# Kernel optimization log

Measured on AMD Instinct MI355X. Metric: run time of the kernel, lower is better.

The kernel has to match this reference:

```python
import jax, jax.numpy as jnp
import numpy as np

B, T, I, H, K, C, TH, CLS = 128, 512, 300, 150, 6, 300, 20, 5

def setup_inputs() -> dict:
    key = jax.random.key(0)
    ks = jax.random.split(key, 16)
    s = lambda *sh: 1.0 / np.sqrt(sh[-1])
    inp = {
        "x": jax.random.normal(ks[0], (B, T, I), jnp.float32),
        # GRU params (PyTorch layout: [3H, in]) for fwd/bwd directions
        "Wih_f": jax.random.normal(ks[1], (3 * H, I), jnp.float32) * s(3 * H, I),
        "Whh_f": jax.random.normal(ks[2], (3 * H, H), jnp.float32) * s(3 * H, H),
        "bih_f": jax.random.normal(ks[3], (3 * H,), jnp.float32) * 0.01,
        "bhh_f": jax.random.normal(ks[4], (3 * H,), jnp.float32) * 0.01,
        "Wih_b": jax.random.normal(ks[5], (3 * H, I), jnp.float32) * s(3 * H, I),
        "Whh_b": jax.random.normal(ks[6], (3 * H, H), jnp.float32) * s(3 * H, H),
        "bih_b": jax.random.normal(ks[7], (3 * H,), jnp.float32) * 0.01,
        "bhh_b": jax.random.normal(ks[8], (3 * H,), jnp.float32) * 0.01,
        # topic attention params (stacked over K topics)
        "attn_context": jax.random.normal(ks[9], (K, C), jnp.float32),
        "Wattn": jax.random.normal(ks[10], (K, C + 2 * H, 2 * H), jnp.float32) * s(1, C + 2 * H),
        "battn": jax.random.normal(ks[11], (K, 2 * H), jnp.float32) * 0.01,
        "Wtop": jax.random.normal(ks[12], (K, 2 * H, TH), jnp.float32) * s(1, 2 * H),
        "btop": jax.random.normal(ks[13], (K, TH), jnp.float32) * 0.01,
        "Wout": jax.random.normal(ks[14], (K * TH, CLS), jnp.float32) * s(1, K * TH),
        "bout": jax.random.normal(ks[15], (CLS,), jnp.float32) * 0.01,
    }
    return inp

def _gru_dir(x, Wih, Whh, bih, bhh, reverse):
    # x: [B,T,I] -> outputs [B,T,H], final hidden [B,H]
    xT = jnp.swapaxes(x, 0, 1)                    # [T,B,I]
    if reverse:
        xT = xT[::-1]
    gi = xT @ Wih.T + bih                         # [T,B,3H] input projections (one big GEMM)
    h0 = jnp.zeros((x.shape[0], Whh.shape[1]), x.dtype)
    def step(h, g):
        gh = h @ Whh.T + bhh
        i_r, i_z, i_n = jnp.split(g, 3, axis=-1)
        h_r, h_z, h_n = jnp.split(gh, 3, axis=-1)
        r = jax.nn.sigmoid(i_r + h_r)
        z = jax.nn.sigmoid(i_z + h_z)
        n = jnp.tanh(i_n + r * h_n)
        h_new = (1.0 - z) * n + z * h
        return h_new, h_new
    hT, ys = jax.lax.scan(step, h0, gi)
    if reverse:
        ys = ys[::-1]
    return jnp.swapaxes(ys, 0, 1), hT

def reference(x, Wih_f, Whh_f, bih_f, bhh_f, Wih_b, Whh_b, bih_b, bhh_b,
              attn_context, Wattn, battn, Wtop, btop, Wout, bout):
    # eval mode: dropout is identity
    out_f, h_f = _gru_dir(x, Wih_f, Whh_f, bih_f, bhh_f, False)
    out_b, h_b = _gru_dir(x, Wih_b, Whh_b, bih_b, bhh_b, True)
    seq = jnp.concatenate([out_f, out_b], axis=-1)       # [B,T,2H]
    hidden = jnp.concatenate([h_f, h_b], axis=-1)        # [B,2H]
    Bsz = x.shape[0]
    Kt = attn_context.shape[0]
    # per-topic context: cat(context_k, hidden) -> linear -> tanh, batched over topics
    ctx_in = jnp.concatenate([
        jnp.broadcast_to(attn_context[None, :, :], (Bsz, Kt, attn_context.shape[1])),
        jnp.broadcast_to(hidden[:, None, :], (Bsz, Kt, hidden.shape[1])),
    ], axis=-1)                                          # [B,K,C+2H]
    context = jnp.tanh(jnp.einsum('bkc,kcd->bkd', ctx_in, Wattn) + battn)  # [B,K,2H]
    # attention pooling over time, all topics at once
    energy = jnp.einsum('btd,bkd->btk', seq, context)    # [B,T,K]
    probs = jax.nn.softmax(energy, axis=1)
    pooled = jnp.einsum('btd,btk->bkd', seq, probs)      # [B,K,2H]
    topic = jax.nn.relu(jnp.einsum('bkd,kdh->bkh', pooled, Wtop) + btop)   # [B,K,TH]
    feats = topic.reshape(Bsz, -1)                       # [B,K*TH]
    logits = feats @ Wout + bout
    out = jax.nn.softmax(logits, axis=1)                 # eval + validate=False path
    # regularization loss on normalized contexts
    nc = context / jnp.linalg.norm(context, axis=2, keepdims=True).clip(1e-12)
    G = jnp.einsum('bkd,bjd->bkj', nc, nc)               # [B,K,K]
    diff = G - jnp.eye(Kt, dtype=G.dtype)[None]
    reg = jnp.mean(jnp.sqrt(jnp.sum(diff * diff, axis=(1, 2))))
    return out, reg
```

## Files before the change

kernel.cpp:

```cpp
#include <hip/hip_runtime.h>
#include <hip/hip_bf16.h>
#include <math.h>

#define Bq   128
#define Tq   512
#define Iq   300
#define Hq   150
#define G3   450
#define Kq   6
#define Cq   300
#define D2   300
#define THq  20
#define CLSq 5

typedef __attribute__((ext_vector_type(8))) short short8;
typedef __attribute__((ext_vector_type(4))) float floatx4;

__global__ __launch_bounds__(256) void cast_bf16_kernel(
    const float* __restrict__ in, __hip_bfloat16* __restrict__ out, int n4)
{
    const int i = blockIdx.x * 256 + threadIdx.x;
    if (i < n4) {
        float4 v = *(const float4*)(in + 4 * (size_t)i);
        out[4 * (size_t)i + 0] = __float2bfloat16(v.x);
        out[4 * (size_t)i + 1] = __float2bfloat16(v.y);
        out[4 * (size_t)i + 2] = __float2bfloat16(v.z);
        out[4 * (size_t)i + 3] = __float2bfloat16(v.w);
    }
}

#define LB 40

__global__ __launch_bounds__(256) void gi_gemm_mfma(
    const __hip_bfloat16* __restrict__ xb,
    const __hip_bfloat16* __restrict__ Wbf,
    const float* __restrict__ bf_, const float* __restrict__ bb_,
    float* __restrict__ gic, int t0f, int t0b, int tcShift)
{
    const int dir = blockIdx.z;
    const unsigned short* W = (const unsigned short*)(Wbf + (size_t)dir * G3 * Iq);
    const unsigned short* X = (const unsigned short*)xb;
    const float* bias = dir ? bb_ : bf_;
    const int t0 = dir ? t0b : t0f;
    const int TCr = 1 << tcShift;
    float* outb = gic + (size_t)dir * Bq * TCr * G3;

    const int m0 = blockIdx.y * 128;
    const int n0 = blockIdx.x * 128;
    const int tid  = threadIdx.x;
    const int wv   = tid >> 6, lane = tid & 63;
    const int wm   = wv & 1,  wn   = wv >> 1;
    const int quad = lane >> 4, mr = lane & 15;

    __shared__ __align__(16) unsigned short Ab[128 * LB];
    __shared__ __align__(16) unsigned short Bb[128 * LB];

    floatx4 acc[4][4];
    #pragma unroll
    for (int i = 0; i < 4; ++i)
        #pragma unroll
        for (int j = 0; j < 4; ++j)
            acc[i][j] = (floatx4){0.f, 0.f, 0.f, 0.f};

    for (int k0 = 0; k0 < 320; k0 += 32) {
        __syncthreads();
        #pragma unroll
        for (int i = 0; i < 4; ++i) {
            const int g = tid + 256 * i;
            const int row = g >> 3, kq = g & 7;
            const int k = k0 + kq * 4;
            const int r = m0 + row;
            const int bb2 = r >> tcShift, lt = r & (TCr - 1);
            ushort4 av = make_ushort4(0, 0, 0, 0);
            if (k < Iq)
                av = *(const ushort4*)(X + ((size_t)bb2 * Tq + t0 + lt) * Iq + k);
            *(ushort4*)&Ab[row * LB + kq * 4] = av;
            const int n = n0 + row;
            ushort4 bv = make_ushort4(0, 0, 0, 0);
            if (n < G3 && k < Iq)
                bv = *(const ushort4*)(W + (size_t)n * Iq + k);
            *(ushort4*)&Bb[row * LB + kq * 4] = bv;
        }
        __syncthreads();

        short8 af[4], bfr[4];
        #pragma unroll
        for (int i = 0; i < 4; ++i)
            af[i] = *(const short8*)&Ab[(wm * 64 + i * 16 + mr) * LB + quad * 8];
        #pragma unroll
        for (int j = 0; j < 4; ++j)
            bfr[j] = *(const short8*)&Bb[(wn * 64 + j * 16 + mr) * LB + quad * 8];
        #pragma unroll
        for (int i = 0; i < 4; ++i)
            #pragma unroll
            for (int j = 0; j < 4; ++j)
                acc[i][j] = __builtin_amdgcn_mfma_f32_16x16x32_bf16(
                    af[i], bfr[j], acc[i][j], 0, 0, 0);
    }

    #pragma unroll
    for (int j = 0; j < 4; ++j) {
        const int gn = n0 + wn * 64 + j * 16 + mr;
        if (gn >= G3) continue;
        const float bv = bias[gn];
        #pragma unroll
        for (int i = 0; i < 4; ++i) {
            const int mbase = m0 + wm * 64 + i * 16 + quad * 4;
            #pragma unroll
            for (int rg = 0; rg < 4; ++rg)
                outb[(size_t)(mbase + rg) * G3 + gn] = acc[i][j][rg] + bv;
        }
    }
}

__global__ __launch_bounds__(512, 2) void gru_rec(
    const float* __restrict__ gic,
    const float* __restrict__ Whh_f, const float* __restrict__ bhh_f,
    const float* __restrict__ Whh_b, const float* __restrict__ bhh_b,
    float* __restrict__ hstate,
    float* __restrict__ seq,
    int chunk, int tcShift)
{
    const int TCr = 1 << tcShift;
    const int bid = blockIdx.x;
    const int dir = bid & 1;
    const int b   = bid >> 1;
    const float* Whh = dir ? Whh_b : Whh_f;
    const float* bhh = dir ? bhh_b : bhh_f;
    const int tid = threadIdx.x;
    const int rq  = tid >> 2;
    const int p   = tid & 3;
    const bool gact = (rq < 113);
    const bool iact = (tid < 450);

    __shared__ __align__(16) float stage[64 * 150];
    __shared__ __align__(16) float4 hbuf4[40];
    __shared__ __align__(16) float ghp[4][456];
    __shared__ float gi_s[456];
    float* hbuf = (float*)hbuf4;

    float w[4][40];

    for (int c = 0; c < 8; ++c) {
        const int r0 = c * 64;
        const int nrows = (r0 + 64 <= G3) ? 64 : (G3 - r0);
        const int nel = nrows * 150;
        __syncthreads();
        for (int idx = tid * 4; idx < nel; idx += 512 * 4)
            *(float4*)&stage[idx] = *(const float4*)(Whh + (size_t)r0 * 150 + idx);
        __syncthreads();
        if (gact && (rq >> 4) == c) {
            const int rl = 4 * rq - r0;
            const int cmax = (p == 3) ? 36 : 38;
            #pragma unroll
            for (int r = 0; r < 4; ++r) {
                const bool rv = (4 * rq + r < G3);
                #pragma unroll
                for (int cc = 0; cc < 40; ++cc)
                    w[r][cc] = (rv && cc < cmax)
                             ? stage[(rl + r) * 150 + p * 38 + cc] : 0.f;
            }
        }
    }

    float bh3[3] = {0.f, 0.f, 0.f};
    if (tid < Hq) {
        bh3[0] = bhh[tid];
        bh3[1] = bhh[150 + tid];
        bh3[2] = bhh[300 + tid];
    }
    const int hslot = (tid / 38) * 40 + (tid % 38);

    float* hs = hstate + (size_t)(dir * Bq + b) * Hq;
    if (tid < 160) {
        const int pp = tid / 40, off = tid % 40;
        const int j = pp * 38 + off;
        hbuf[tid] = (off < 38 && j < Hq && chunk > 0) ? hs[j] : 0.f;
    }
    __syncthreads();

    const float* gib = gic + (size_t)(dir * Bq + b) * TCr * G3;
    const int t0 = dir ? (Tq - TCr * (chunk + 1)) : (chunk * TCr);
    float* seqb = seq + (size_t)b * Tq * D2 + dir * Hq;

    int lt = dir ? (TCr - 1) : 0;
    float gval = iact ? gib[(size_t)lt * G3 + tid] : 0.f;

    for (int s = 0; s < TCr; ++s) {
        const int ltn = dir ? (TCr - 2 - s) : (s + 1);
        float gnext = 0.f;
        if (s + 1 < TCr && iact)
            gnext = gib[(size_t)ltn * G3 + tid];

        if (iact) gi_s[tid] = gval;

        if (gact) {
            const float4* hh = hbuf4 + p * 10;
            float acc0 = 0.f, acc1 = 0.f, acc2 = 0.f, acc3 = 0.f;
            #pragma unroll
            for (int q = 0; q < 10; ++q) {
                const float4 hv = hh[q];
                acc0 += hv.x * w[0][4*q]   + hv.y * w[0][4*q+1]
                      + hv.z * w[0][4*q+2] + hv.w * w[0][4*q+3];
                acc1 += hv.x * w[1][4*q]   + hv.y * w[1][4*q+1]
                      + hv.z * w[1][4*q+2] + hv.w * w[1][4*q+3];
                acc2 += hv.x * w[2][4*q]   + hv.y * w[2][4*q+1]
                      + hv.z * w[2][4*q+2] + hv.w * w[2][4*q+3];
                acc3 += hv.x * w[3][4*q]   + hv.y * w[3][4*q+1]
                      + hv.z * w[3][4*q+2] + hv.w * w[3][4*q+3];
            }
            *(float4*)&ghp[p][4 * rq] = make_float4(acc0, acc1, acc2, acc3);
        }
        __syncthreads();

        if (tid < Hq) {
            const float ghr = ghp[0][tid] + ghp[1][tid]
                            + ghp[2][tid] + ghp[3][tid] + bh3[0];
            const float ghz = ghp[0][150+tid] + ghp[1][150+tid]
                            + ghp[2][150+tid] + ghp[3][150+tid] + bh3[1];
            const float ghn = ghp[0][300+tid] + ghp[1][300+tid]
                            + ghp[2][300+tid] + ghp[3][300+tid] + bh3[2];
            const float r = 1.f / (1.f + __expf(-(gi_s[tid]       + ghr)));
            const float z = 1.f / (1.f + __expf(-(gi_s[150 + tid] + ghz)));
            const float nv = tanhf(gi_s[300 + tid] + r * ghn);
            const float hn = (1.f - z) * nv + z * hbuf[hslot];
            hbuf[hslot] = hn;
            stage[(s & 63) * 150 + tid] = hn;
        }
        __syncthreads();

        if ((s & 63) == 63 || s == TCr - 1) {
            const int sf0 = s & ~63;
            const int nf2 = (s - sf0 + 1) * 75;
            for (int idx = tid; idx < nf2; idx += 512) {
                const int rrow = idx / 75, cc = idx % 75;
                const int ss = sf0 + rrow;
                const int ltw = dir ? (TCr - 1 - ss) : ss;
                *(float2*)(seqb + (size_t)(t0 + ltw) * D2 + 2 * cc) =
                    *(const float2*)&stage[rrow * 150 + 2 * cc];
            }
        }

        gval = gnext;
        lt = ltn;
    }

    if (tid < Hq) hs[tid] = hbuf[hslot];
}

__global__ void ctxw_kernel(
    const float* __restrict__ attn_context,
    const float* __restrict__ Wattn,
    const float* __restrict__ battn,
    float* __restrict__ ctxW)
{
    const int o = blockIdx.x * 256 + threadIdx.x;
    if (o >= Kq * D2) return;
    const int k = o / D2, d = o % D2;
    float acc = battn[o];
    const float* Wp = Wattn + ((size_t)k * (Cq + D2)) * D2 + d;
    for (int c = 0; c < Cq; ++c)
        acc += attn_context[k * Cq + c] * Wp[(size_t)c * D2];
    ctxW[o] = acc;
}

__global__ __launch_bounds__(256) void ctx_compute(
    const float* __restrict__ seq,
    const float* __restrict__ Wattn,
    const float* __restrict__ ctxW,
    float* __restrict__ context,
    float* __restrict__ normsq)
{
    const int b = blockIdx.x;
    const int k = blockIdx.y;
    const int tid = threadIdx.x;
    const int lane = tid & 63, wv = tid >> 6;

    __shared__ float hb[304];
    __shared__ float red[4];

    for (int i = tid; i < D2; i += 256)
        hb[i] = (i < Hq) ? seq[((size_t)b * Tq + (Tq - 1)) * D2 + i]
                         : seq[(size_t)b * Tq * D2 + i];
    __syncthreads();

    float ssq = 0.f;
    for (int d = tid; d < D2; d += 256) {
        float acc = ctxW[k * D2 + d];
        const float* Wp = Wattn + ((size_t)k * (Cq + D2) + Cq) * D2 + d;
        for (int jj = 0; jj < D2; ++jj)
            acc += hb[jj] * Wp[(size_t)jj * D2];
        const float c = tanhf(acc);
        context[((size_t)b * Kq + k) * D2 + d] = c;
        ssq += c * c;
    }
    for (int off = 32; off > 0; off >>= 1) ssq += __shfl_xor(ssq, off, 64);
    if (lane == 0) red[wv] = ssq;
    __syncthreads();
    if (tid == 0) normsq[b * Kq + k] = red[0] + red[1] + red[2] + red[3];
}

__global__ __launch_bounds__(256) void gram_kernel(
    const float* __restrict__ context,
    const float* __restrict__ normsq,
    float* __restrict__ regbuf)
{
    const int b = blockIdx.x;
    const int tid = threadIdx.x;
    __shared__ float ctx[Kq * D2];
    __shared__ float Gm[36];

    for (int o = tid; o < Kq * D2; o += 256)
        ctx[o] = context[(size_t)b * Kq * D2 + o];
    __syncthreads();

    if (tid < 36) {
        const int k = tid / 6, jj = tid % 6;
        float g = 0.f;
        for (int d = 0; d < D2; ++d)
            g += ctx[k * D2 + d] * ctx[jj * D2 + d];
        const float nk = fmaxf(sqrtf(normsq[b * Kq + k]), 1e-12f);
        const float nj = fmaxf(sqrtf(normsq[b * Kq + jj]), 1e-12f);
        g /= (nk * nj);
        const float diff = g - ((k == jj) ? 1.f : 0.f);
        Gm[tid] = diff * diff;
    }
    __syncthreads();
    if (tid == 0) {
        float s = 0.f;
        for (int i = 0; i < 36; ++i) s += Gm[i];
        regbuf[b] = sqrtf(s);
    }
}

__global__ __launch_bounds__(256) void energy_kernel(
    const float* __restrict__ seq,
    const float* __restrict__ context,
    float* __restrict__ en)
{
    const int tc = blockIdx.x;
    const int b  = blockIdx.y;
    const int tid = threadIdx.x;
    const int lane = tid & 63, wv = tid >> 6;

    __shared__ float ctx[Kq * D2];
    for (int o = tid; o < Kq * D2; o += 256)
        ctx[o] = context[(size_t)b * Kq * D2 + o];
    __syncthreads();

    const float* seqb = seq + (size_t)b * Tq * D2;
    for (int s = 0; s < 16; ++s) {
        const int tt = tc * 64 + s * 4 + wv;
        float acc[Kq] = {0.f,0.f,0.f,0.f,0.f,0.f};
        for (int d = lane; d < D2; d += 64) {
            const float sv = seqb[(size_t)tt * D2 + d];
            #pragma unroll
            for (int k = 0; k < Kq; ++k) acc[k] += sv * ctx[k * D2 + d];
        }
        #pragma unroll
        for (int k = 0; k < Kq; ++k) {
            float v = acc[k];
            for (int off = 32; off > 0; off >>= 1) v += __shfl_xor(v, off, 64);
            if (lane == 0) en[((size_t)b * Tq + tt) * Kq + k] = v;
        }
    }
}

__global__ __launch_bounds__(256) void softmax_kernel(float* __restrict__ en)
{
    const int b = blockIdx.x;
    const int tid = threadIdx.x;
    const int lane = tid & 63, wv = tid >> 6;
    __shared__ float es[Tq * Kq];
    __shared__ float red[8];

    for (int o = tid; o < Tq * Kq; o += 256)
        es[o] = en[(size_t)b * Tq * Kq + o];
    __syncthreads();

    for (int k = 0; k < Kq; ++k) {
        float m = -1e30f;
        for (int tt = tid; tt < Tq; tt += 256) m = fmaxf(m, es[tt * Kq + k]);
        for (int off = 32; off > 0; off >>= 1) m = fmaxf(m, __shfl_xor(m, off, 64));
        if (lane == 0) red[wv] = m;
        __syncthreads();
        m = fmaxf(fmaxf(red[0], red[1]), fmaxf(red[2], red[3]));
        float ssum = 0.f;
        for (int tt = tid; tt < Tq; tt += 256) {
            const float e = __expf(es[tt * Kq + k] - m);
            es[tt * Kq + k] = e;
            ssum += e;
        }
        for (int off = 32; off > 0; off >>= 1) ssum += __shfl_xor(ssum, off, 64);
        if (lane == 0) red[4 + wv] = ssum;
        __syncthreads();
        const float inv = 1.f / (red[4] + red[5] + red[6] + red[7]);
        for (int tt = tid; tt < Tq; tt += 256) es[tt * Kq + k] *= inv;
        __syncthreads();
    }

    for (int o = tid; o < Tq * Kq; o += 256)
        en[(size_t)b * Tq * Kq + o] = es[o];
}

__global__ __launch_bounds__(256) void pooledp_kernel(
    const float* __restrict__ seq,
    const float* __restrict__ en,
    float* __restrict__ partial)
{
    const int tc = blockIdx.x;
    const int b  = blockIdx.y;
    const int tid = threadIdx.x;
    const int lane = tid & 63, wv = tid >> 6;

    __shared__ float pr[64 * Kq];
    __shared__ float part[4][Kq * D2];

    if (tid < 64 * Kq / 2) {
        pr[tid]       = en[((size_t)b * Tq + tc * 64) * Kq + tid];
        pr[tid + 192] = en[((size_t)b * Tq + tc * 64) * Kq + tid + 192];
    }
    __syncthreads();

    const float* seqb = seq + (size_t)b * Tq * D2;

    float pp[Kq][5];
    #pragma unroll
    for (int k = 0; k < Kq; ++k)
        #pragma unroll
        for (int q = 0; q < 5; ++q) pp[k][q] = 0.f;

    for (int s = 0; s < 16; ++s) {
        const int tl = s * 4 + wv;
        const int tt = tc * 64 + tl;
        float prr[Kq];
        #pragma unroll
        for (int k = 0; k < Kq; ++k) prr[k] = pr[tl * Kq + k];
        #pragma unroll
        for (int q = 0; q < 5; ++q) {
            const int d = lane + q * 64;
            const float sv = (d < D2) ? seqb[(size_t)tt * D2 + d] : 0.f;
            #pragma unroll
            for (int k = 0; k < Kq; ++k) pp[k][q] += prr[k] * sv;
        }
    }
    #pragma unroll
    for (int k = 0; k < Kq; ++k)
        #pragma unroll
        for (int q = 0; q < 5; ++q) {
            const int d = lane + q * 64;
            if (d < D2) part[wv][k * D2 + d] = pp[k][q];
        }
    __syncthreads();
    float* op = partial + ((size_t)b * 8 + tc) * (Kq * D2);
    for (int o = tid; o < Kq * D2; o += 256)
        op[o] = part[0][o] + part[1][o] + part[2][o] + part[3][o];
}

__global__ __launch_bounds__(256) void final_kernel(
    const float* __restrict__ partial,
    const float* __restrict__ Wtop,
    const float* __restrict__ btop,
    const float* __restrict__ Wout,
    const float* __restrict__ bout,
    float* __restrict__ outp)
{
    const int b = blockIdx.x;
    const int tid = threadIdx.x;
    __shared__ float pooled[Kq * D2];
    __shared__ float feats[Kq * THq];
    __shared__ float lsm[8];

    for (int o = tid; o < Kq * D2; o += 256) {
        float s = 0.f;
        #pragma unroll
        for (int c = 0; c < 8; ++c)
            s += partial[((size_t)b * 8 + c) * (Kq * D2) + o];
        pooled[o] = s;
    }
    __syncthreads();

    if (tid < Kq * THq) {
        const int k = tid / THq, hh = tid % THq;
        float acc = btop[tid];
        const float* wp = Wtop + (size_t)k * D2 * THq + hh;
        for (int d = 0; d < D2; ++d)
            acc += pooled[k * D2 + d] * wp[(size_t)d * THq];
        feats[tid] = fmaxf(acc, 0.f);
    }
    __syncthreads();

    if (tid < CLSq) {
        float acc = bout[tid];
        for (int f = 0; f < Kq * THq; ++f)
            acc += feats[f] * Wout[f * CLSq + tid];
        lsm[tid] = acc;
    }
    __syncthreads();
    if (tid < CLSq) {
        float m = lsm[0];
        for (int c = 1; c < CLSq; ++c) m = fmaxf(m, lsm[c]);
        float s = 0.f;
        for (int c = 0; c < CLSq; ++c) s += __expf(lsm[c] - m);
        outp[(size_t)b * CLSq + tid] = __expf(lsm[tid] - m) / s;
    }
}

__global__ void reg_final(const float* __restrict__ regbuf, float* __restrict__ outp)
{
    const int tid = threadIdx.x;
    float v = regbuf[tid];
    for (int off = 32; off > 0; off >>= 1) v += __shfl_xor(v, off, 64);
    __shared__ float r2[2];
    if ((tid & 63) == 0) r2[tid >> 6] = v;
    __syncthreads();
    if (tid == 0) outp[Bq * CLSq] = (r2[0] + r2[1]) * (1.f / (float)Bq);
}

extern "C" void kernel_launch(void* const* d_in, const int* in_sizes, int n_in,
                              void* d_out, int out_size, void* d_ws, size_t ws_size,
                              hipStream_t stream)
{
    const float* x     = (const float*)d_in[0];
    const float* Wih_f = (const float*)d_in[1];
    const float* Whh_f = (const float*)d_in[2];
    const float* bih_f = (const float*)d_in[3];
    const float* bhh_f = (const float*)d_in[4];
    const float* Wih_b = (const float*)d_in[5];
    const float* Whh_b = (const float*)d_in[6];
    const float* bih_b = (const float*)d_in[7];
    const float* bhh_b = (const float*)d_in[8];
    const float* attn_context = (const float*)d_in[9];
    const float* Wattn = (const float*)d_in[10];
    const float* battn = (const float*)d_in[11];
    const float* Wtop  = (const float*)d_in[12];
    const float* btop  = (const float*)d_in[13];
    const float* Wout  = (const float*)d_in[14];
    const float* bout  = (const float*)d_in[15];
    float* outp = (float*)d_out;

    float* ws       = (float*)d_ws;
    float* seqv     = ws;
    float* hstate   = seqv + (size_t)Bq * Tq * D2;
    float* ctxW     = hstate + (size_t)2 * Bq * Hq;
    float* context  = ctxW + Kq * D2;
    float* regbuf   = context + (size_t)Bq * Kq * D2;
    float* normsq   = regbuf + Bq;
    float* en       = normsq + Bq * Kq;
    float* partial  = en + (size_t)Bq * Tq * Kq;
    __hip_bfloat16* xb16 = (__hip_bfloat16*)(partial + (size_t)Bq * 8 * Kq * D2);
    __hip_bfloat16* Wb16 = xb16 + (size_t)Bq * Tq * Iq;
    float* gi_chunk = (float*)(Wb16 + (size_t)2 * G3 * Iq);
    const size_t fixed_floats = (size_t)(gi_chunk - ws);

    int tcShift = 5;
    for (int sh = 8; sh >= 5; --sh) {
        size_t need = (fixed_floats + (size_t)115200 * (1 << sh)) * 4;
        if (need <= ws_size) { tcShift = sh; break; }
    }
    const int TCr = 1 << tcShift;
    const int NL = Tq / TCr;

    cast_bf16_kernel<<<dim3((Bq * Tq * Iq / 4 + 255) / 256), 256, 0, stream>>>(
        x, xb16, Bq * Tq * Iq / 4);
    cast_bf16_kernel<<<dim3((G3 * Iq / 4 + 255) / 256), 256, 0, stream>>>(
        Wih_f, Wb16, G3 * Iq / 4);
    cast_bf16_kernel<<<dim3((G3 * Iq / 4 + 255) / 256), 256, 0, stream>>>(
        Wih_b, Wb16 + (size_t)G3 * Iq, G3 * Iq / 4);

    for (int c = 0; c < NL; ++c) {
        const int t0f = c * TCr;
        const int t0b = Tq - TCr * (c + 1);
        gi_gemm_mfma<<<dim3(4, Bq * TCr / 128, 2), 256, 0, stream>>>(
            xb16, Wb16, bih_f, bih_b, gi_chunk, t0f, t0b, tcShift);
        gru_rec<<<dim3(2 * Bq), 512, 0, stream>>>(
            gi_chunk, Whh_f, bhh_f, Whh_b, bhh_b, hstate, seqv, c, tcShift);
    }

    ctxw_kernel<<<dim3((Kq * D2 + 255) / 256), 256, 0, stream>>>(
        attn_context, Wattn, battn, ctxW);
    ctx_compute<<<dim3(Bq, Kq), 256, 0, stream>>>(seqv, Wattn, ctxW, context, normsq);
    gram_kernel<<<dim3(Bq), 256, 0, stream>>>(context, normsq, regbuf);
    energy_kernel<<<dim3(8, Bq), 256, 0, stream>>>(seqv, context, en);
    softmax_kernel<<<dim3(Bq), 256, 0, stream>>>(en);
    pooledp_kernel<<<dim3(8, Bq), 256, 0, stream>>>(seqv, en, partial);
    final_kernel<<<dim3(Bq), 256, 0, stream>>>(partial, Wtop, btop, Wout, bout, outp);
    reg_final<<<dim3(1), 128, 0, stream>>>(regbuf, outp);
}
```

Before: 1.047 ms.

## Fuse bf16 cast into GEMM loads, use fp16 dot2 recurrence with burst gi prefetch

Removes the separate bf16 cast kernels and converts x and Wih to bf16 while loading them inside the MFMA GEMM. In the recurrent kernel, Whh is held in registers as packed fp16 pairs and the hidden state is mirrored in fp16 so the matvec uses fdot2, halving register weight storage and the FMA count. Input-gate projections are now prefetched into shared memory in double-buffered bursts of 8 timesteps instead of one per-step global load, and the seq flush granularity drops to 32 steps. The fp16 hidden state and weights reduce accuracy in the recurrence, and the extra shared memory may affect occupancy.

```diff
diff --git a/kernel.cpp b/kernel.cpp
--- a/kernel.cpp
+++ b/kernel.cpp
@@ -15,31 +15,33 @@
 
 typedef __attribute__((ext_vector_type(8))) short short8;
 typedef __attribute__((ext_vector_type(4))) float floatx4;
-
-__global__ __launch_bounds__(256) void cast_bf16_kernel(
-    const float* __restrict__ in, __hip_bfloat16* __restrict__ out, int n4)
-{
-    const int i = blockIdx.x * 256 + threadIdx.x;
-    if (i < n4) {
-        float4 v = *(const float4*)(in + 4 * (size_t)i);
-        out[4 * (size_t)i + 0] = __float2bfloat16(v.x);
-        out[4 * (size_t)i + 1] = __float2bfloat16(v.y);
-        out[4 * (size_t)i + 2] = __float2bfloat16(v.z);
-        out[4 * (size_t)i + 3] = __float2bfloat16(v.w);
-    }
+typedef __attribute__((ext_vector_type(2))) _Float16 half2_t;
+
+static __device__ __forceinline__ unsigned short f2bf(float f) {
+    unsigned int u = __builtin_bit_cast(unsigned int, f);
+    u += 0x7FFFu + ((u >> 16) & 1u);
+    return (unsigned short)(u >> 16);
+}
+
+static __device__ __forceinline__ float dot2f(half2_t a, half2_t b, float c) {
+#if __has_builtin(__builtin_amdgcn_fdot2)
+    return __builtin_amdgcn_fdot2(a, b, c, false);
+#else
+    return c + (float)a.x * (float)b.x + (float)a.y * (float)b.y;
+#endif
 }
 
 #define LB 40
 
 __global__ __launch_bounds__(256) void gi_gemm_mfma(
-    const __hip_bfloat16* __restrict__ xb,
-    const __hip_bfloat16* __restrict__ Wbf,
+    const float* __restrict__ x,
+    const float* __restrict__ Wf_,
+    const float* __restrict__ Wb_,
     const float* __restrict__ bf_, const float* __restrict__ bb_,
     float* __restrict__ gic, int t0f, int t0b, int tcShift)
 {
     const int dir = blockIdx.z;
-    const unsigned short* W = (const unsigned short*)(Wbf + (size_t)dir * G3 * Iq);
-    const unsigned short* X = (const unsigned short*)xb;
+    const float* W    = dir ? Wb_ : Wf_;
     const float* bias = dir ? bb_ : bf_;
     const int t0 = dir ? t0b : t0f;
     const int TCr = 1 << tcShift;
@@ -72,13 +74,17 @@
             const int r = m0 + row;
             const int bb2 = r >> tcShift, lt = r & (TCr - 1);
             ushort4 av = make_ushort4(0, 0, 0, 0);
-            if (k < Iq)
-                av = *(const ushort4*)(X + ((size_t)bb2 * Tq + t0 + lt) * Iq + k);
+            if (k < Iq) {
+                float4 v = *(const float4*)(x + ((size_t)bb2 * Tq + t0 + lt) * Iq + k);
+                av = make_ushort4(f2bf(v.x), f2bf(v.y), f2bf(v.z), f2bf(v.w));
+            }
             *(ushort4*)&Ab[row * LB + kq * 4] = av;
             const int n = n0 + row;
             ushort4 bv = make_ushort4(0, 0, 0, 0);
-            if (n < G3 && k < Iq)
-                bv = *(const ushort4*)(W + (size_t)n * Iq + k);
+            if (n < G3 && k < Iq) {
+                float4 v = *(const float4*)(W + (size_t)n * Iq + k);
+                bv = make_ushort4(f2bf(v.x), f2bf(v.y), f2bf(v.z), f2bf(v.w));
+            }
             *(ushort4*)&Bb[row * LB + kq * 4] = bv;
         }
         __syncthreads();
@@ -131,34 +137,44 @@
     const int rq  = tid >> 2;
     const int p   = tid & 3;
     const bool gact = (rq < 113);
-    const bool iact = (tid < 450);
-
-    __shared__ __align__(16) float stage[64 * 150];
-    __shared__ __align__(16) float4 hbuf4[40];
+
+    __shared__ __align__(16) float stage[32 * 150];
+    __shared__ __align__(16) float gib_s[2][8 * 450];
     __shared__ __align__(16) float ghp[4][456];
-    __shared__ float gi_s[456];
-    float* hbuf = (float*)hbuf4;
-
-    float w[4][40];
-
-    for (int c = 0; c < 8; ++c) {
-        const int r0 = c * 64;
-        const int nrows = (r0 + 64 <= G3) ? 64 : (G3 - r0);
+    __shared__ __align__(16) unsigned short h16[160];
+    __shared__ float h32[152];
+
+    half2_t w[4][20];
+    #pragma unroll
+    for (int r = 0; r < 4; ++r)
+        #pragma unroll
+        for (int c = 0; c < 20; ++c)
+            w[r][c] = (half2_t)(_Float16)0.f;
+
+    for (int c = 0; c < 15; ++c) {
+        const int r0 = c * 32;
+        const int nrows = (r0 + 32 <= G3) ? 32 : (G3 - r0);
         const int nel = nrows * 150;
         __syncthreads();
         for (int idx = tid * 4; idx < nel; idx += 512 * 4)
             *(float4*)&stage[idx] = *(const float4*)(Whh + (size_t)r0 * 150 + idx);
         __syncthreads();
-        if (gact && (rq >> 4) == c) {
+        if (gact && (rq >> 3) == c) {
             const int rl = 4 * rq - r0;
-            const int cmax = (p == 3) ? 36 : 38;
+            const int cmax2 = (p == 3) ? 18 : 19;
             #pragma unroll
             for (int r = 0; r < 4; ++r) {
                 const bool rv = (4 * rq + r < G3);
                 #pragma unroll
-                for (int cc = 0; cc < 40; ++cc)
-                    w[r][cc] = (rv && cc < cmax)
-                             ? stage[(rl + r) * 150 + p * 38 + cc] : 0.f;
+                for (int cc = 0; cc < 19; ++cc) {
+                    float f0 = 0.f, f1 = 0.f;
+                    if (rv && cc < cmax2) {
+                        f0 = stage[(rl + r) * 150 + p * 38 + 2 * cc];
+                        f1 = stage[(rl + r) * 150 + p * 38 + 2 * cc + 1];
+                    }
+                    half2_t hw; hw.x = (_Float16)f0; hw.y = (_Float16)f1;
+                    w[r][cc] = hw;
+                }
             }
         }
     }
@@ -169,50 +185,69 @@
         bh3[1] = bhh[150 + tid];
         bh3[2] = bhh[300 + tid];
     }
-    const int hslot = (tid / 38) * 40 + (tid % 38);
+    const int pq = tid / 38;
+    const int h16slot = pq * 40 + (tid - pq * 38);
 
     float* hs = hstate + (size_t)(dir * Bq + b) * Hq;
     if (tid < 160) {
-        const int pp = tid / 40, off = tid % 40;
-        const int j = pp * 38 + off;
-        hbuf[tid] = (off < 38 && j < Hq && chunk > 0) ? hs[j] : 0.f;
-    }
-    __syncthreads();
+        const int pp = tid / 40, cc = tid % 40;
+        const int cmax = (pp == 3) ? 36 : 38;
+        const int j = pp * 38 + cc;
+        float v = (cc < cmax && chunk > 0) ? hs[j] : 0.f;
+        h16[tid] = __builtin_bit_cast(unsigned short, (_Float16)v);
+    }
+    if (tid < Hq) h32[tid] = (chunk > 0) ? hs[tid] : 0.f;
 
     const float* gib = gic + (size_t)(dir * Bq + b) * TCr * G3;
     const int t0 = dir ? (Tq - TCr * (chunk + 1)) : (chunk * TCr);
     float* seqb = seq + (size_t)b * Tq * D2 + dir * Hq;
 
-    int lt = dir ? (TCr - 1) : 0;
-    float gval = iact ? gib[(size_t)lt * G3 + tid] : 0.f;
+    auto load_burst = [&](int sb, int buf) {
+        #pragma unroll
+        for (int i = 0; i < 8; ++i) {
+            const int idx = tid + i * 512;
+            if (idx < 3600) {
+                const int ss = idx / 450;
+                const int j  = idx - ss * 450;
+                const int lt = dir ? (TCr - 1 - (sb + ss)) : (sb + ss);
+                gib_s[buf][ss * 450 + j] = gib[(size_t)lt * G3 + j];
+            }
+        }
+    };
+    load_burst(0, 0);
+    __syncthreads();
 
     for (int s = 0; s < TCr; ++s) {
-        const int ltn = dir ? (TCr - 2 - s) : (s + 1);
-        float gnext = 0.f;
-        if (s + 1 < TCr && iact)
-            gnext = gib[(size_t)ltn * G3 + tid];
-
-        if (iact) gi_s[tid] = gval;
+        if ((s & 7) == 0 && s + 8 < TCr)
+            load_burst(s + 8, ((s >> 3) + 1) & 1);
 
         if (gact) {
-            const float4* hh = hbuf4 + p * 10;
-            float acc0 = 0.f, acc1 = 0.f, acc2 = 0.f, acc3 = 0.f;
+            const float4* hq = (const float4*)((const unsigned char*)h16 + p * 80);
+            const float4 q0 = hq[0], q1 = hq[1], q2 = hq[2], q3 = hq[3], q4 = hq[4];
+            half2_t hh[20];
+            hh[0]=__builtin_bit_cast(half2_t,q0.x); hh[1]=__builtin_bit_cast(half2_t,q0.y);
+            hh[2]=__builtin_bit_cast(half2_t,q0.z); hh[3]=__builtin_bit_cast(half2_t,q0.w);
+            hh[4]=__builtin_bit_cast(half2_t,q1.x); hh[5]=__builtin_bit_cast(half2_t,q1.y);
+            hh[6]=__builtin_bit_cast(half2_t,q1.z); hh[7]=__builtin_bit_cast(half2_t,q1.w);
+            hh[8]=__builtin_bit_cast(half2_t,q2.x); hh[9]=__builtin_bit_cast(half2_t,q2.y);
+            hh[10]=__builtin_bit_cast(half2_t,q2.z); hh[11]=__builtin_bit_cast(half2_t,q2.w);
+            hh[12]=__builtin_bit_cast(half2_t,q3.x); hh[13]=__builtin_bit_cast(half2_t,q3.y);
+            hh[14]=__builtin_bit_cast(half2_t,q3.z); hh[15]=__builtin_bit_cast(half2_t,q3.w);
+            hh[16]=__builtin_bit_cast(half2_t,q4.x); hh[17]=__builtin_bit_cast(half2_t,q4.y);
+            hh[18]=__builtin_bit_cast(half2_t,q4.z); hh[19]=__builtin_bit_cast(half2_t,q4.w);
+            float a0 = 0.f, a1 = 0.f, a2 = 0.f, a3 = 0.f;
             #pragma unroll
-            for (int q = 0; q < 10; ++q) {
-                const float4 hv = hh[q];
-                acc0 += hv.x * w[0][4*q]   + hv.y * w[0][4*q+1]
-                      + hv.z * w[0][4*q+2] + hv.w * w[0][4*q+3];
-                acc1 += hv.x * w[1][4*q]   + hv.y * w[1][4*q+1]
-                      + hv.z * w[1][4*q+2] + hv.w * w[1][4*q+3];
-                acc2 += hv.x * w[2][4*q]   + hv.y * w[2][4*q+1]
-                      + hv.z * w[2][4*q+2] + hv.w * w[2][4*q+3];
-                acc3 += hv.x * w[3][4*q]   + hv.y * w[3][4*q+1]
-                      + hv.z * w[3][4*q+2] + hv.w * w[3][4*q+3];
+            for (int k = 0; k < 20; ++k) {
+                a0 = dot2f(w[0][k], hh[k], a0);
+                a1 = dot2f(w[1][k], hh[k], a1);
+                a2 = dot2f(w[2][k], hh[k], a2);
+                a3 = dot2f(w[3][k], hh[k], a3);
             }
-            *(float4*)&ghp[p][4 * rq] = make_float4(acc0, acc1, acc2, acc3);
-        }
-        __syncthreads();
-
+            *(float4*)&ghp[p][4 * rq] = make_float4(a0, a1, a2, a3);
+        }
+        __syncthreads();
+
+        const float* gi_row = &gib_s[(s >> 3) & 1][(s & 7) * 450];
         if (tid < Hq) {
             const float ghr = ghp[0][tid] + ghp[1][tid]
                             + ghp[2][tid] + ghp[3][tid] + bh3[0];
@@ -220,32 +255,30 @@
                             + ghp[2][150+tid] + ghp[3][150+tid] + bh3[1];
             const float ghn = ghp[0][300+tid] + ghp[1][300+tid]
                             + ghp[2][300+tid] + ghp[3][300+tid] + bh3[2];
-            const float r = 1.f / (1.f + __expf(-(gi_s[tid]       + ghr)));
-            const float z = 1.f / (1.f + __expf(-(gi_s[150 + tid] + ghz)));
-            const float nv = tanhf(gi_s[300 + tid] + r * ghn);
-            const float hn = (1.f - z) * nv + z * hbuf[hslot];
-            hbuf[hslot] = hn;
-            stage[(s & 63) * 150 + tid] = hn;
-        }
-        __syncthreads();
-
-        if ((s & 63) == 63 || s == TCr - 1) {
-            const int sf0 = s & ~63;
+            const float r = 1.f / (1.f + __expf(-(gi_row[tid]       + ghr)));
+            const float z = 1.f / (1.f + __expf(-(gi_row[150 + tid] + ghz)));
+            const float nv = tanhf(gi_row[300 + tid] + r * ghn);
+            const float hn = (1.f - z) * nv + z * h32[tid];
+            h32[tid] = hn;
+            h16[h16slot] = __builtin_bit_cast(unsigned short, (_Float16)hn);
+            stage[(s & 31) * 150 + tid] = hn;
+        }
+        __syncthreads();
+
+        if ((s & 31) == 31 || s == TCr - 1) {
+            const int sf0 = s & ~31;
             const int nf2 = (s - sf0 + 1) * 75;
             for (int idx = tid; idx < nf2; idx += 512) {
-                const int rrow = idx / 75, cc = idx % 75;
-                const int ss = sf0 + rrow;
-                const int ltw = dir ? (TCr - 1 - ss) : ss;
+                const int rrow = idx / 75, cc = idx - rrow * 75;
+                const int ssg = sf0 + rrow;
+                const int ltw = dir ? (TCr - 1 - ssg) : ssg;
                 *(float2*)(seqb + (size_t)(t0 + ltw) * D2 + 2 * cc) =
                     *(const float2*)&stage[rrow * 150 + 2 * cc];
             }
         }
-
-        gval = gnext;
-        lt = ltn;
-    }
-
-    if (tid < Hq) hs[tid] = hbuf[hslot];
+    }
+
+    if (tid < Hq) hs[tid] = h32[tid];
 }
 
 __global__ void ctxw_kernel(
@@ -548,9 +581,7 @@
     float* normsq   = regbuf + Bq;
     float* en       = normsq + Bq * Kq;
     float* partial  = en + (size_t)Bq * Tq * Kq;
-    __hip_bfloat16* xb16 = (__hip_bfloat16*)(partial + (size_t)Bq * 8 * Kq * D2);
-    __hip_bfloat16* Wb16 = xb16 + (size_t)Bq * Tq * Iq;
-    float* gi_chunk = (float*)(Wb16 + (size_t)2 * G3 * Iq);
+    float* gi_chunk = partial + (size_t)Bq * 8 * Kq * D2;
     const size_t fixed_floats = (size_t)(gi_chunk - ws);
 
     int tcShift = 5;
@@ -561,18 +592,11 @@
     const int TCr = 1 << tcShift;
     const int NL = Tq / TCr;
 
-    cast_bf16_kernel<<<dim3((Bq * Tq * Iq / 4 + 255) / 256), 256, 0, stream>>>(
-        x, xb16, Bq * Tq * Iq / 4);
-    cast_bf16_kernel<<<dim3((G3 * Iq / 4 + 255) / 256), 256, 0, stream>>>(
-        Wih_f, Wb16, G3 * Iq / 4);
-    cast_bf16_kernel<<<dim3((G3 * Iq / 4 + 255) / 256), 256, 0, stream>>>(
-        Wih_b, Wb16 + (size_t)G3 * Iq, G3 * Iq / 4);
-
     for (int c = 0; c < NL; ++c) {
         const int t0f = c * TCr;
         const int t0b = Tq - TCr * (c + 1);
         gi_gemm_mfma<<<dim3(4, Bq * TCr / 128, 2), 256, 0, stream>>>(
-            xb16, Wb16, bih_f, bih_b, gi_chunk, t0f, t0b, tcShift);
+            x, Wih_f, Wih_b, bih_f, bih_b, gi_chunk, t0f, t0b, tcShift);
         gru_rec<<<dim3(2 * Bq), 512, 0, stream>>>(
             gi_chunk, Whh_f, bhh_f, Whh_b, bhh_b, hstate, seqv, c, tcShift);
     }
```

Result: slower. 1.196 ms (+14.2%).
